# Performance work log

Measured on AMD Instinct MI355X. Metric: run time of the kernel, lower is better.

Reference implementation:

```python
import jax, jax.numpy as jnp
import numpy as np


def setup_inputs() -> dict:
    key = jax.random.key(0)
    ks = jax.random.split(key, 7)
    B, P, S, I, H, O = 8, 32, 2048, 32, 64, 32
    return {
        "x": jax.random.normal(ks[0], (B, P, S, I), dtype=jnp.float32),
        "W_ih": jax.random.normal(ks[1], (H, I), dtype=jnp.float32) * 0.1,
        "b_ih": jax.random.normal(ks[2], (H,), dtype=jnp.float32) * 0.1,
        "W_hh": jax.random.normal(ks[3], (H, H), dtype=jnp.float32) * 0.1,
        "b_hh": jax.random.normal(ks[4], (H,), dtype=jnp.float32) * 0.1,
        "W_fc": jax.random.normal(ks[5], (O, H), dtype=jnp.float32) * 0.1,
        "b_fc": jax.random.normal(ks[6], (O,), dtype=jnp.float32) * 0.1,
    }


def reference(x, W_ih, b_ih, W_hh, b_hh, W_fc, b_fc):
    # x: [B, P, S, I] (batch, num_particles, seq_len, input_size)
    B, P, S, I = x.shape
    H = W_hh.shape[0]
    # Precompute the input-to-hidden projection for all timesteps at once.
    # pre: [S, B, P, H]
    pre = jnp.einsum('bpsi,hi->sbph', x, W_ih) + b_ih + b_hh
    h0 = jnp.zeros((B, P, H), dtype=x.dtype)

    def step(hx, pre_t):
        # hx: [B, P, H]; pre_t: [B, P, H]
        hy = jnp.tanh(pre_t + jnp.einsum('bph,gh->bpg', hx, W_hh))
        return hy, hy

    h_last, hs = jax.lax.scan(step, h0, pre)  # hs: [S, B, P, H]
    hidden = jnp.moveaxis(hs, 0, 2)           # [B, P, S, H]
    # sigma_y == 0 -> add_noise is a no-op; observations are just the fc output
    observations = jnp.einsum('bpsh,oh->bpso', hidden, W_fc) + b_fc  # [B, P, S, O]
    return observations, hidden, h_last
```

## Files before the change

kernel.cpp:

```cpp
#include <hip/hip_runtime.h>

#define S_LEN 2048
#define I_IN  32
#define H_DIM 64
#define O_DIM 32
#define NSEQ  256
#define NROWS (NSEQ * S_LEN)
#define OBS_ELEMS (NROWS * O_DIM)
#define HID_ELEMS (NROWS * H_DIM)

__global__ __launch_bounds__(256) void pre_kernel(
    const float* __restrict__ x,
    const float* __restrict__ Wih,
    const float* __restrict__ bih,
    const float* __restrict__ bhh,
    float* __restrict__ pre)
{
    __shared__ float ws[I_IN][68];
    __shared__ float bsh[H_DIM];

    const int tid = threadIdx.x;
#pragma unroll
    for (int s = 0; s < 8; ++s) {
        const int e = tid + 256 * s;
        ws[e & 31][e >> 5] = Wih[e];
    }
    if (tid < H_DIM) bsh[tid] = bih[tid] + bhh[tid];
    __syncthreads();

    const int r    = tid & 127;
    const int half = tid >> 7;
    const size_t row = (size_t)blockIdx.x * 128 + r;
    const int o0 = half * 32;

    float4 xr[8];
    const float4* xg = (const float4*)(x + row * I_IN);
#pragma unroll
    for (int k = 0; k < 8; ++k) xr[k] = xg[k];

    float4 acc[8];
#pragma unroll
    for (int j = 0; j < 8; ++j) acc[j] = *(const float4*)&bsh[o0 + 4 * j];

#pragma unroll
    for (int k = 0; k < 8; ++k) {
        const float xi0 = xr[k].x, xi1 = xr[k].y, xi2 = xr[k].z, xi3 = xr[k].w;
#pragma unroll
        for (int j = 0; j < 8; ++j) {
            const float4 w0 = *(const float4*)&ws[4 * k + 0][o0 + 4 * j];
            const float4 w1 = *(const float4*)&ws[4 * k + 1][o0 + 4 * j];
            const float4 w2 = *(const float4*)&ws[4 * k + 2][o0 + 4 * j];
            const float4 w3 = *(const float4*)&ws[4 * k + 3][o0 + 4 * j];
            acc[j].x = fmaf(xi0, w0.x, acc[j].x);
            acc[j].y = fmaf(xi0, w0.y, acc[j].y);
            acc[j].z = fmaf(xi0, w0.z, acc[j].z);
            acc[j].w = fmaf(xi0, w0.w, acc[j].w);
            acc[j].x = fmaf(xi1, w1.x, acc[j].x);
            acc[j].y = fmaf(xi1, w1.y, acc[j].y);
            acc[j].z = fmaf(xi1, w1.z, acc[j].z);
            acc[j].w = fmaf(xi1, w1.w, acc[j].w);
            acc[j].x = fmaf(xi2, w2.x, acc[j].x);
            acc[j].y = fmaf(xi2, w2.y, acc[j].y);
            acc[j].z = fmaf(xi2, w2.z, acc[j].z);
            acc[j].w = fmaf(xi2, w2.w, acc[j].w);
            acc[j].x = fmaf(xi3, w3.x, acc[j].x);
            acc[j].y = fmaf(xi3, w3.y, acc[j].y);
            acc[j].z = fmaf(xi3, w3.z, acc[j].z);
            acc[j].w = fmaf(xi3, w3.w, acc[j].w);
        }
    }

    float4* pr = (float4*)(pre + row * H_DIM + o0);
#pragma unroll
    for (int j = 0; j < 8; ++j) pr[j] = acc[j];
}

__device__ __forceinline__ float rl(float v, int l)
{
    return __int_as_float(__builtin_amdgcn_readlane(__float_as_int(v), l));
}

__device__ __forceinline__ float rnn_step(float pv, float hv, const float* whh)
{
    float z0 = pv, z1 = 0.0f, z2 = 0.0f, z3 = 0.0f;
    float z4 = 0.0f, z5 = 0.0f, z6 = 0.0f, z7 = 0.0f;
#pragma unroll
    for (int h = 0; h < H_DIM; h += 8) {
        z0 = fmaf(whh[h + 0], rl(hv, h + 0), z0);
        z1 = fmaf(whh[h + 1], rl(hv, h + 1), z1);
        z2 = fmaf(whh[h + 2], rl(hv, h + 2), z2);
        z3 = fmaf(whh[h + 3], rl(hv, h + 3), z3);
        z4 = fmaf(whh[h + 4], rl(hv, h + 4), z4);
        z5 = fmaf(whh[h + 5], rl(hv, h + 5), z5);
        z6 = fmaf(whh[h + 6], rl(hv, h + 6), z6);
        z7 = fmaf(whh[h + 7], rl(hv, h + 7), z7);
    }
    const float z = ((z0 + z1) + (z2 + z3)) + ((z4 + z5) + (z6 + z7));
    const float e = __expf(2.0f * z);
    return fmaf(-2.0f, __builtin_amdgcn_rcpf(e + 1.0f), 1.0f);
}

__global__ __launch_bounds__(64, 1) void rnn_scan_kernel(
    const float* __restrict__ Whh,
    float* __restrict__ hidden,
    float* __restrict__ hlast)
{
    const int q = blockIdx.x;
    const int g = threadIdx.x;

    float whh[H_DIM];
#pragma unroll
    for (int h = 0; h < H_DIM; ++h) whh[h] = Whh[g * H_DIM + h];

    float* hq = hidden + (size_t)q * S_LEN * H_DIM;

    float hv = 0.0f;
    float buf[8];
#pragma unroll
    for (int j = 0; j < 8; ++j) buf[j] = hq[j * H_DIM + g];

    for (int tb = 0; tb < S_LEN - 8; tb += 8) {
        float nbuf[8];
#pragma unroll
        for (int j = 0; j < 8; ++j) nbuf[j] = hq[(tb + 8 + j) * H_DIM + g];
#pragma unroll
        for (int j = 0; j < 8; ++j) {
            hv = rnn_step(buf[j], hv, whh);
            hq[(tb + j) * H_DIM + g] = hv;
        }
#pragma unroll
        for (int j = 0; j < 8; ++j) buf[j] = nbuf[j];
    }
#pragma unroll
    for (int j = 0; j < 8; ++j) {
        hv = rnn_step(buf[j], hv, whh);
        hq[(S_LEN - 8 + j) * H_DIM + g] = hv;
    }

    hlast[q * H_DIM + g] = hv;
}

__global__ __launch_bounds__(256) void obs_kernel(
    const float* __restrict__ hidden,
    const float* __restrict__ Wfc,
    const float* __restrict__ bfc,
    float* __restrict__ obs)
{
    __shared__ float wt[H_DIM][36];
    __shared__ float bsh[O_DIM];

    const int tid = threadIdx.x;
#pragma unroll
    for (int s = 0; s < 8; ++s) {
        const int e = tid + 256 * s;
        wt[e & 63][e >> 6] = Wfc[e];
    }
    if (tid < O_DIM) bsh[tid] = bfc[tid];
    __syncthreads();

    const int r    = tid & 127;
    const int half = tid >> 7;
    const size_t row = (size_t)blockIdx.x * 128 + r;
    const int o0 = half * 16;

    float4 hr[16];
    const float4* hg = (const float4*)(hidden + row * H_DIM);
#pragma unroll
    for (int k = 0; k < 16; ++k) hr[k] = hg[k];

    float4 acc[4];
#pragma unroll
    for (int j = 0; j < 4; ++j) acc[j] = *(const float4*)&bsh[o0 + 4 * j];

#pragma unroll
    for (int k = 0; k < 16; ++k) {
        const float h0 = hr[k].x, h1 = hr[k].y, h2 = hr[k].z, h3 = hr[k].w;
#pragma unroll
        for (int j = 0; j < 4; ++j) {
            const float4 w0 = *(const float4*)&wt[4 * k + 0][o0 + 4 * j];
            const float4 w1 = *(const float4*)&wt[4 * k + 1][o0 + 4 * j];
            const float4 w2 = *(const float4*)&wt[4 * k + 2][o0 + 4 * j];
            const float4 w3 = *(const float4*)&wt[4 * k + 3][o0 + 4 * j];
            acc[j].x = fmaf(h0, w0.x, acc[j].x);
            acc[j].y = fmaf(h0, w0.y, acc[j].y);
            acc[j].z = fmaf(h0, w0.z, acc[j].z);
            acc[j].w = fmaf(h0, w0.w, acc[j].w);
            acc[j].x = fmaf(h1, w1.x, acc[j].x);
            acc[j].y = fmaf(h1, w1.y, acc[j].y);
            acc[j].z = fmaf(h1, w1.z, acc[j].z);
            acc[j].w = fmaf(h1, w1.w, acc[j].w);
            acc[j].x = fmaf(h2, w2.x, acc[j].x);
            acc[j].y = fmaf(h2, w2.y, acc[j].y);
            acc[j].z = fmaf(h2, w2.z, acc[j].z);
            acc[j].w = fmaf(h2, w2.w, acc[j].w);
            acc[j].x = fmaf(h3, w3.x, acc[j].x);
            acc[j].y = fmaf(h3, w3.y, acc[j].y);
            acc[j].z = fmaf(h3, w3.z, acc[j].z);
            acc[j].w = fmaf(h3, w3.w, acc[j].w);
        }
    }

    float4* op = (float4*)(obs + row * O_DIM + o0);
#pragma unroll
    for (int j = 0; j < 4; ++j) op[j] = acc[j];
}

extern "C" void kernel_launch(void* const* d_in, const int* in_sizes, int n_in,
                              void* d_out, int out_size, void* d_ws, size_t ws_size,
                              hipStream_t stream)
{
    const float* x   = (const float*)d_in[0];
    const float* Wih = (const float*)d_in[1];
    const float* bih = (const float*)d_in[2];
    const float* Whh = (const float*)d_in[3];
    const float* bhh = (const float*)d_in[4];
    const float* Wfc = (const float*)d_in[5];
    const float* bfc = (const float*)d_in[6];

    float* out    = (float*)d_out;
    float* obs    = out;
    float* hidden = out + (size_t)OBS_ELEMS;
    float* hlast  = hidden + (size_t)HID_ELEMS;

    pre_kernel<<<NROWS / 128, 256, 0, stream>>>(x, Wih, bih, bhh, hidden);
    rnn_scan_kernel<<<NSEQ, 64, 0, stream>>>(Whh, hidden, hlast);
    obs_kernel<<<NROWS / 128, 256, 0, stream>>>(hidden, Wfc, bfc, obs);
}
```

Baseline: 801.8 us.

## Stage input rows in LDS and hold weight rows in registers for projections

Both pre_kernel and obs_kernel are restructured. Each block now stages its 128 input rows into LDS with coalesced float4 loads, and each thread keeps one weight row in registers, computing one output column across many rows. Before, every thread loaded its own row from global memory with strided float4 accesses and streamed the transposed weights from LDS. The new layout gives coalesced global loads and broadcast LDS reads, but writes become scalar per-column stores, and the LDS footprint grows (32 KB for obs), which may lower occupancy.

```diff
diff --git a/kernel.cpp b/kernel.cpp
--- a/kernel.cpp
+++ b/kernel.cpp
@@ -16,63 +16,44 @@
     const float* __restrict__ bhh,
     float* __restrict__ pre)
 {
-    __shared__ float ws[I_IN][68];
-    __shared__ float bsh[H_DIM];
+    __shared__ float4 xs4[1024];
 
     const int tid = threadIdx.x;
+    const size_t row0 = (size_t)blockIdx.x * 128;
+
+    const float4* xg = (const float4*)(x + row0 * I_IN);
 #pragma unroll
-    for (int s = 0; s < 8; ++s) {
-        const int e = tid + 256 * s;
-        ws[e & 31][e >> 5] = Wih[e];
+    for (int s = 0; s < 4; ++s) xs4[tid + 256 * s] = xg[tid + 256 * s];
+
+    const int g = tid & 63;
+    float wih[I_IN];
+    const float4* wg = (const float4*)(Wih + g * I_IN);
+#pragma unroll
+    for (int k = 0; k < 8; ++k) {
+        const float4 wv = wg[k];
+        wih[4 * k + 0] = wv.x; wih[4 * k + 1] = wv.y;
+        wih[4 * k + 2] = wv.z; wih[4 * k + 3] = wv.w;
     }
-    if (tid < H_DIM) bsh[tid] = bih[tid] + bhh[tid];
+    const float bias = bih[g] + bhh[g];
+
     __syncthreads();
 
-    const int r    = tid & 127;
-    const int half = tid >> 7;
-    const size_t row = (size_t)blockIdx.x * 128 + r;
-    const int o0 = half * 32;
-
-    float4 xr[8];
-    const float4* xg = (const float4*)(x + row * I_IN);
+    const int w = tid >> 6;
+#pragma unroll 2
+    for (int j = 0; j < 32; ++j) {
+        const int r = w * 32 + j;
+        const float4* xr = &xs4[r * 8];
+        float a0 = bias, a1 = 0.0f, a2 = 0.0f, a3 = 0.0f;
 #pragma unroll
-    for (int k = 0; k < 8; ++k) xr[k] = xg[k];
-
-    float4 acc[8];
-#pragma unroll
-    for (int j = 0; j < 8; ++j) acc[j] = *(const float4*)&bsh[o0 + 4 * j];
-
-#pragma unroll
-    for (int k = 0; k < 8; ++k) {
-        const float xi0 = xr[k].x, xi1 = xr[k].y, xi2 = xr[k].z, xi3 = xr[k].w;
-#pragma unroll
-        for (int j = 0; j < 8; ++j) {
-            const float4 w0 = *(const float4*)&ws[4 * k + 0][o0 + 4 * j];
-            const float4 w1 = *(const float4*)&ws[4 * k + 1][o0 + 4 * j];
-            const float4 w2 = *(const float4*)&ws[4 * k + 2][o0 + 4 * j];
-            const float4 w3 = *(const float4*)&ws[4 * k + 3][o0 + 4 * j];
-            acc[j].x = fmaf(xi0, w0.x, acc[j].x);
-            acc[j].y = fmaf(xi0, w0.y, acc[j].y);
-            acc[j].z = fmaf(xi0, w0.z, acc[j].z);
-            acc[j].w = fmaf(xi0, w0.w, acc[j].w);
-            acc[j].x = fmaf(xi1, w1.x, acc[j].x);
-            acc[j].y = fmaf(xi1, w1.y, acc[j].y);
-            acc[j].z = fmaf(xi1, w1.z, acc[j].z);
-            acc[j].w = fmaf(xi1, w1.w, acc[j].w);
-            acc[j].x = fmaf(xi2, w2.x, acc[j].x);
-            acc[j].y = fmaf(xi2, w2.y, acc[j].y);
-            acc[j].z = fmaf(xi2, w2.z, acc[j].z);
-            acc[j].w = fmaf(xi2, w2.w, acc[j].w);
-            acc[j].x = fmaf(xi3, w3.x, acc[j].x);
-            acc[j].y = fmaf(xi3, w3.y, acc[j].y);
-            acc[j].z = fmaf(xi3, w3.z, acc[j].z);
-            acc[j].w = fmaf(xi3, w3.w, acc[j].w);
+        for (int k = 0; k < 8; ++k) {
+            const float4 xb = xr[k];
+            a0 = fmaf(wih[4 * k + 0], xb.x, a0);
+            a1 = fmaf(wih[4 * k + 1], xb.y, a1);
+            a2 = fmaf(wih[4 * k + 2], xb.z, a2);
+            a3 = fmaf(wih[4 * k + 3], xb.w, a3);
         }
+        pre[(row0 + r) * H_DIM + g] = (a0 + a1) + (a2 + a3);
     }
-
-    float4* pr = (float4*)(pre + row * H_DIM + o0);
-#pragma unroll
-    for (int j = 0; j < 8; ++j) pr[j] = acc[j];
 }
 
 __device__ __forceinline__ float rl(float v, int l)
@@ -146,63 +127,45 @@
     const float* __restrict__ bfc,
     float* __restrict__ obs)
 {
-    __shared__ float wt[H_DIM][36];
-    __shared__ float bsh[O_DIM];
+    __shared__ float4 hs4[2048];
 
     const int tid = threadIdx.x;
+    const size_t row0 = (size_t)blockIdx.x * 128;
+
+    const float4* hg = (const float4*)(hidden + row0 * H_DIM);
 #pragma unroll
-    for (int s = 0; s < 8; ++s) {
-        const int e = tid + 256 * s;
-        wt[e & 63][e >> 6] = Wfc[e];
+    for (int s = 0; s < 8; ++s) hs4[tid + 256 * s] = hg[tid + 256 * s];
+
+    const int o  = tid & 31;
+    const int hi = (tid >> 5) & 1;
+    float wfc[H_DIM];
+    const float4* wg = (const float4*)(Wfc + o * H_DIM);
+#pragma unroll
+    for (int k = 0; k < 16; ++k) {
+        const float4 wv = wg[k];
+        wfc[4 * k + 0] = wv.x; wfc[4 * k + 1] = wv.y;
+        wfc[4 * k + 2] = wv.z; wfc[4 * k + 3] = wv.w;
     }
-    if (tid < O_DIM) bsh[tid] = bfc[tid];
+    const float bias = bfc[o];
+
     __syncthreads();
 
-    const int r    = tid & 127;
-    const int half = tid >> 7;
-    const size_t row = (size_t)blockIdx.x * 128 + r;
-    const int o0 = half * 16;
-
-    float4 hr[16];
-    const float4* hg = (const float4*)(hidden + row * H_DIM);
+    const int w = tid >> 6;
+#pragma unroll 2
+    for (int j = 0; j < 16; ++j) {
+        const int r = w * 32 + 2 * j + hi;
+        const float4* hr = &hs4[r * 16];
+        float a0 = bias, a1 = 0.0f, a2 = 0.0f, a3 = 0.0f;
 #pragma unroll
-    for (int k = 0; k < 16; ++k) hr[k] = hg[k];
-
-    float4 acc[4];
-#pragma unroll
-    for (int j = 0; j < 4; ++j) acc[j] = *(const float4*)&bsh[o0 + 4 * j];
-
-#pragma unroll
-    for (int k = 0; k < 16; ++k) {
-        const float h0 = hr[k].x, h1 = hr[k].y, h2 = hr[k].z, h3 = hr[k].w;
-#pragma unroll
-        for (int j = 0; j < 4; ++j) {
-            const float4 w0 = *(const float4*)&wt[4 * k + 0][o0 + 4 * j];
-            const float4 w1 = *(const float4*)&wt[4 * k + 1][o0 + 4 * j];
-            const float4 w2 = *(const float4*)&wt[4 * k + 2][o0 + 4 * j];
-            const float4 w3 = *(const float4*)&wt[4 * k + 3][o0 + 4 * j];
-            acc[j].x = fmaf(h0, w0.x, acc[j].x);
-            acc[j].y = fmaf(h0, w0.y, acc[j].y);
-            acc[j].z = fmaf(h0, w0.z, acc[j].z);
-            acc[j].w = fmaf(h0, w0.w, acc[j].w);
-            acc[j].x = fmaf(h1, w1.x, acc[j].x);
-            acc[j].y = fmaf(h1, w1.y, acc[j].y);
-            acc[j].z = fmaf(h1, w1.z, acc[j].z);
-            acc[j].w = fmaf(h1, w1.w, acc[j].w);
-            acc[j].x = fmaf(h2, w2.x, acc[j].x);
-            acc[j].y = fmaf(h2, w2.y, acc[j].y);
-            acc[j].z = fmaf(h2, w2.z, acc[j].z);
-            acc[j].w = fmaf(h2, w2.w, acc[j].w);
-            acc[j].x = fmaf(h3, w3.x, acc[j].x);
-            acc[j].y = fmaf(h3, w3.y, acc[j].y);
-            acc[j].z = fmaf(h3, w3.z, acc[j].z);
-            acc[j].w = fmaf(h3, w3.w, acc[j].w);
+        for (int k = 0; k < 16; ++k) {
+            const float4 hb = hr[k];
+            a0 = fmaf(wfc[4 * k + 0], hb.x, a0);
+            a1 = fmaf(wfc[4 * k + 1], hb.y, a1);
+            a2 = fmaf(wfc[4 * k + 2], hb.z, a2);
+            a3 = fmaf(wfc[4 * k + 3], hb.w, a3);
         }
+        obs[(row0 + r) * O_DIM + o] = (a0 + a1) + (a2 + a3);
     }
-
-    float4* op = (float4*)(obs + row * O_DIM + o0);
-#pragma unroll
-    for (int j = 0; j < 4; ++j) op[j] = acc[j];
 }
 
 extern "C" void kernel_launch(void* const* d_in, const int* in_sizes, int n_in,
```

After: 797.8 us. About the same (-0.5%).
